# Optimization experiments

Hardware: AMD Instinct MI355X
Metric: run time of the kernel (lower is better)

Reference implementation:

```python
import jax, jax.numpy as jnp
import numpy as np


def _mlp(h, W1, b1, W2, b2):
    # Linear -> ReLU -> Linear
    h = jax.nn.relu(h @ W1 + b1)
    return h @ W2 + b2


def setup_inputs() -> dict:
    key = jax.random.key(0)
    ks = jax.random.split(key, 8)
    N, E, DN, DE, H, O = 50000, 800000, 128, 64, 256, 128
    DIN = DN + DE  # 192
    s1 = 1.0 / np.sqrt(DIN)
    s2 = 1.0 / np.sqrt(H)
    return {
        "x": jax.random.normal(ks[0], (N, DN), dtype=jnp.float32),
        "edge_index": jax.random.randint(ks[1], (2, E), 0, N, dtype=jnp.int32),
        "edge_attr": jax.random.normal(ks[2], (E, DE), dtype=jnp.float32),
        "W1_out": jax.random.normal(ks[3], (DIN, H), dtype=jnp.float32) * s1,
        "b1_out": jnp.zeros((H,), dtype=jnp.float32),
        "W2_out": jax.random.normal(ks[4], (H, O), dtype=jnp.float32) * s2,
        "b2_out": jnp.zeros((O,), dtype=jnp.float32),
        "W1_in": jax.random.normal(ks[5], (DIN, H), dtype=jnp.float32) * s1,
        "b1_in": jnp.zeros((H,), dtype=jnp.float32),
        "W2_in": jax.random.normal(ks[6], (H, O), dtype=jnp.float32) * s2,
        "b2_in": jnp.zeros((O,), dtype=jnp.float32),
    }


def reference(x, edge_index, edge_attr, W1_out, b1_out, W2_out, b2_out,
              W1_in, b1_in, W2_in, b2_in):
    N = x.shape[0]
    row, col = edge_index[0], edge_index[1]
    # Shared gather + concat: [E, d_node + d_edge]
    msg_in = jnp.concatenate([x[col], edge_attr], axis=1)

    # flow_out: edges with row < col. Compute MLP densely, zero masked edges,
    # then scatter-sum -> identical math to masked gather + scatter-sum.
    m_out = (row < col).astype(x.dtype)[:, None]
    flow_out = _mlp(msg_in, W1_out, b1_out, W2_out, b2_out) * m_out
    flow_out = jax.ops.segment_sum(flow_out, row, num_segments=N)

    # flow_in: edges with row > col
    m_in = (row > col).astype(x.dtype)[:, None]
    flow_in = _mlp(msg_in, W1_in, b1_in, W2_in, b2_in) * m_in
    flow_in = jax.ops.segment_sum(flow_in, row, num_segments=N)

    return jnp.concatenate((flow_in, flow_out), axis=1)  # [N, 2*O]
```

## Files before the change

### kernel.cpp

```cpp
#include <hip/hip_runtime.h>
#include <hip/hip_bf16.h>

typedef __attribute__((ext_vector_type(8))) short short8;
typedef __attribute__((ext_vector_type(8))) unsigned short ushort8;
typedef __attribute__((ext_vector_type(4))) float f32x4;
typedef __attribute__((ext_vector_type(2))) unsigned int uint2v;
typedef __attribute__((ext_vector_type(4))) unsigned int uint4v;

#define DN   128
#define DE   64
#define DIN  192
#define HID  256
#define OUTD 128
#define TE   64
#define NT   256
#define MSG_LD 200
#define OUT_LD 132
#define NMB  (TE / 16)

static __device__ __forceinline__ unsigned short f2b(float f) {
    unsigned int u = __float_as_uint(f);
    u += 0x7fffu + ((u >> 16) & 1u);
    return (unsigned short)(u >> 16);
}

static __device__ __forceinline__ unsigned int cvt_pk2(float lo, float hi) {
    unsigned int r;
    asm("v_cvt_pk_bf16_f32 %0, %1, %2" : "=v"(r) : "v"(lo), "v"(hi));
    return r;
}

template<int OFF>
static __device__ __forceinline__ uint2v tr_read(unsigned addr) {
    uint2v d;
    asm volatile("ds_read_b64_tr_b16 %0, %1 offset:%c2"
                 : "=v"(d) : "v"(addr), "n"(OFF));
    return d;
}

__global__ __launch_bounds__(256)
void prep_kernel(const float* __restrict__ W1o, const float* __restrict__ W1i,
                 const float* __restrict__ W2o, const float* __restrict__ W2i,
                 unsigned short* __restrict__ W1po, unsigned short* __restrict__ W1pi,
                 unsigned short* __restrict__ W2po, unsigned short* __restrict__ W2pi,
                 const int* __restrict__ ei, int E, int N, int* __restrict__ hist,
                 const float* __restrict__ x, unsigned short* __restrict__ xb) {
    const int S1 = DIN * HID, S2v = HID * OUTD;
    const int PACKN = 2 * S1 + 2 * S2v;
    int idx = blockIdx.x * blockDim.x + threadIdx.x;
    if (idx < PACKN) {
        const float* W; unsigned short* Wp; int Nc, j;
        if      (idx < S1)          { W = W1o; Wp = W1po; Nc = HID;  j = idx; }
        else if (idx < 2*S1)        { W = W1i; Wp = W1pi; Nc = HID;  j = idx - S1; }
        else if (idx < 2*S1 + S2v)  { W = W2o; Wp = W2po; Nc = OUTD; j = idx - 2*S1; }
        else                        { W = W2i; Wp = W2pi; Nc = OUTD; j = idx - 2*S1 - S2v; }
        int k = j / Nc, n = j - k * Nc;
        Wp[(((k >> 5) * Nc + n) << 5) + (k & 31)] = f2b(W[j]);
    } else if (idx < PACKN + E) {
        int e = idx - PACKN;
        int r = ei[e], c = ei[E + e];
        if      (r < c) atomicAdd(&hist[r], 1);
        else if (r > c) atomicAdd(&hist[N + r], 1);
    } else {
        int i = idx - PACKN - E;
        if (i < N * DN / 8) {
            float4 a = reinterpret_cast<const float4*>(x)[i * 2];
            float4 b = reinterpret_cast<const float4*>(x)[i * 2 + 1];
            ushort8 v = { f2b(a.x), f2b(a.y), f2b(a.z), f2b(a.w),
                          f2b(b.x), f2b(b.y), f2b(b.z), f2b(b.w) };
            reinterpret_cast<ushort8*>(xb)[i] = v;
        }
    }
}

__global__ __launch_bounds__(1024)
void scan1_kernel(const int* __restrict__ hist, int* __restrict__ cursor,
                  int* __restrict__ chunkSum, int N, int nch) {
    __shared__ int s_ws[16];
    const int br = blockIdx.x / nch, ch = blockIdx.x - br * nch;
    const int tid = threadIdx.x, lane = tid & 63, wv = tid >> 6;
    const int i = ch * 1024 + tid;
    int v = (i < N) ? hist[(size_t)br * N + i] : 0;
    int incl = v;
    #pragma unroll
    for (int d = 1; d < 64; d <<= 1) {
        int t = __shfl_up(incl, d, 64);
        if (lane >= d) incl += t;
    }
    if (lane == 63) s_ws[wv] = incl;
    __syncthreads();
    if (tid < 16) {
        int w = s_ws[tid];
        int wi = w;
        #pragma unroll
        for (int d = 1; d < 16; d <<= 1) {
            int t = __shfl_up(wi, d, 64);
            if (tid >= d) wi += t;
        }
        s_ws[tid] = wi - w;
    }
    __syncthreads();
    int excl = s_ws[wv] + incl - v;
    if (i < N) cursor[(size_t)br * N + i] = excl;
    if (tid == 1023) chunkSum[br * nch + ch] = excl + v;
}

__global__ __launch_bounds__(128)
void scan2_kernel(int* __restrict__ chunkSum, int* __restrict__ cnt, int nch) {
    const int br = threadIdx.x >> 6, lane = threadIdx.x & 63;
    int v = (lane < nch) ? chunkSum[br * nch + lane] : 0;
    int incl = v;
    #pragma unroll
    for (int d = 1; d < 64; d <<= 1) {
        int t = __shfl_up(incl, d, 64);
        if (lane >= d) incl += t;
    }
    if (lane < nch) chunkSum[br * nch + lane] = incl - v;
    if (lane == nch - 1) cnt[br] = incl;
}

__global__ __launch_bounds__(256)
void reorder_kernel(const int* __restrict__ ei, int E, int N, int nch,
                    int* __restrict__ cursor, const int* __restrict__ chunkSum,
                    int* __restrict__ list_out, int* __restrict__ list_in) {
    int e = blockIdx.x * blockDim.x + threadIdx.x;
    if (e >= E) return;
    int r = ei[e], c = ei[E + e];
    if (r == c) return;
    int br = (r < c) ? 0 : 1;
    int p = chunkSum[br * nch + (r >> 10)] + atomicAdd(&cursor[(size_t)br * N + r], 1);
    (br ? list_in : list_out)[p] = e;
}

__global__ __launch_bounds__(NT, 4)
void mlp_scatter_kernel(const unsigned short* __restrict__ xb,
                        const int* __restrict__ ei,
                        const float* __restrict__ ea,
                        const unsigned short* __restrict__ W1p_out,
                        const unsigned short* __restrict__ W1p_in,
                        const float* __restrict__ b1_out,
                        const float* __restrict__ b1_in,
                        const unsigned short* __restrict__ W2p_out,
                        const unsigned short* __restrict__ W2p_in,
                        const float* __restrict__ b2_out,
                        const float* __restrict__ b2_in,
                        const int* __restrict__ list_out,
                        const int* __restrict__ list_in,
                        const int* __restrict__ cnt,
                        float* __restrict__ out,
                        int E) {
    __shared__ __align__(16) unsigned short s_buf[TE * 264];
    __shared__ int s_eid[TE], s_dest[TE], s_col[TE];

    const int c0 = cnt[0], c1 = cnt[1];
    const int nb0 = (c0 + TE - 1) / TE;
    const int branch = (blockIdx.x >= nb0) ? 1 : 0;
    const int lb = branch ? (blockIdx.x - nb0) : blockIdx.x;
    const int count = branch ? c1 : c0;
    if (lb * TE >= count) return;
    const int* list            = branch ? list_in : list_out;
    const unsigned short* W1p  = branch ? W1p_in  : W1p_out;
    const float* b1            = branch ? b1_in   : b1_out;
    const unsigned short* W2p  = branch ? W2p_in  : W2p_out;
    const float* b2            = branch ? b2_in   : b2_out;
    const int colbase          = branch ? 0 : OUTD;

    const int tid = threadIdx.x;
    if (tid < TE) {
        int idx = lb * TE + tid;
        int e = (idx < count) ? list[idx] : -1;
        s_eid[tid]  = e;
        s_dest[tid] = (e >= 0) ? ei[e] : -1;
        s_col[tid]  = (e >= 0) ? ei[E + e] : 0;
    }
    __syncthreads();

    {
        const int le  = tid >> 2;
        const int sub = tid & 3;
        const int e   = s_eid[le];
        const ushort8* xrow = reinterpret_cast<const ushort8*>(xb) + (size_t)s_col[le] * (DN / 8);
        #pragma unroll
        for (int j = 0; j < 4; ++j) {
            int seg = sub + j * 4;
            ushort8 v = {0, 0, 0, 0, 0, 0, 0, 0};
            if (e >= 0) v = xrow[seg];
            *reinterpret_cast<ushort8*>(&s_buf[le * MSG_LD + seg * 8]) = v;
        }
        const float4* erow = reinterpret_cast<const float4*>(ea) + (size_t)e * (DE / 4);
        #pragma unroll
        for (int j = 0; j < 4; ++j) {
            float4 v = make_float4(0.f, 0.f, 0.f, 0.f);
            if (e >= 0) v = erow[sub * 4 + j];
            unsigned int lo = cvt_pk2(v.x, v.y);
            unsigned int hi = cvt_pk2(v.z, v.w);
            *reinterpret_cast<uint2*>(&s_buf[le * MSG_LD + DN + sub * 16 + j * 4]) = make_uint2(lo, hi);
        }
    }
    __syncthreads();

    const int wave = tid >> 6;
    const int lane = tid & 63;
    const int ln   = lane & 15;
    const int quad = lane >> 4;

    f32x4 acc[4][4];
    {
        const int nbase = wave * 64;
        float bias[4];
        #pragma unroll
        for (int t = 0; t < 4; ++t) bias[t] = b1[nbase + t * 16 + ln];
        #pragma unroll
        for (int mt = 0; mt < 4; ++mt)
            #pragma unroll
            for (int t = 0; t < 4; ++t)
                acc[mt][t] = (f32x4){bias[t], bias[t], bias[t], bias[t]};
        #pragma unroll
        for (int kt = 0; kt < DIN / 32; ++kt) {
            short8 a[4], b[4];
            #pragma unroll
            for (int mt = 0; mt < 4; ++mt)
                a[mt] = *reinterpret_cast<const short8*>(
                    &s_buf[(mt * 16 + ln) * MSG_LD + kt * 32 + quad * 8]);
            #pragma unroll
            for (int t = 0; t < 4; ++t)
                b[t] = *reinterpret_cast<const short8*>(
                    &W1p[((kt * HID + nbase + t * 16 + ln) << 5) + quad * 8]);
            #pragma unroll
            for (int mt = 0; mt < 4; ++mt)
                #pragma unroll
                for (int t = 0; t < 4; ++t)
                    acc[mt][t] = __builtin_amdgcn_mfma_f32_16x16x32_bf16(a[mt], b[t], acc[mt][t], 0, 0, 0);
        }
    }
    __syncthreads();

    {
        const int nbase = wave * 64;
        #pragma unroll
        for (int mt = 0; mt < 4; ++mt)
            #pragma unroll
            for (int t = 0; t < 4; ++t) {
                int n = nbase + t * 16 + ln;
                float r0 = acc[mt][t][0], r1 = acc[mt][t][1];
                float r2 = acc[mt][t][2], r3 = acc[mt][t][3];
                r0 = r0 > 0.f ? r0 : 0.f;  r1 = r1 > 0.f ? r1 : 0.f;
                r2 = r2 > 0.f ? r2 : 0.f;  r3 = r3 > 0.f ? r3 : 0.f;
                unsigned int d0 = cvt_pk2(r0, r1);
                unsigned int d1 = cvt_pk2(r2, r3);
                int el = (((n >> 2) * NMB + mt) << 6) + ((n & 3) << 4) + (quad << 2);
                *reinterpret_cast<uint2v*>(&s_buf[el]) = (uint2v){d0, d1};
            }
    }
    __syncthreads();

    f32x4 acc2[4][2];
    {
        const int nb2 = wave * 32;
        float bz0 = b2[nb2 + ln];
        float bz1 = b2[nb2 + 16 + ln];
        #pragma unroll
        for (int mt = 0; mt < 4; ++mt) {
            acc2[mt][0] = (f32x4){bz0, bz0, bz0, bz0};
            acc2[mt][1] = (f32x4){bz1, bz1, bz1, bz1};
        }
        const unsigned trb = (unsigned)(uintptr_t)(&s_buf[quad * 512 + ln * 4]);
        short8 bn0 = *reinterpret_cast<const short8*>(&W2p[((nb2 + ln) << 5) + quad * 8]);
        short8 bn1 = *reinterpret_cast<const short8*>(&W2p[((nb2 + 16 + ln) << 5) + quad * 8]);

#define G2TR(kt, mt) { \
        uint2v t0 = tr_read<(kt) * 4096 + (mt) * 128>(trb); \
        uint2v t1 = tr_read<(kt) * 4096 + (mt) * 128 + 512>(trb); \
        a[mt] = __builtin_bit_cast(short8, (uint4v){t0.x, t0.y, t1.x, t1.y}); }

#define G2MM(mt) \
        acc2[mt][0] = __builtin_amdgcn_mfma_f32_16x16x32_bf16(a[mt], b0c, acc2[mt][0], 0, 0, 0); \
        acc2[mt][1] = __builtin_amdgcn_mfma_f32_16x16x32_bf16(a[mt], b1c, acc2[mt][1], 0, 0, 0);

#define G2STEP(kt) { \
        short8 a[4]; \
        G2TR(kt, 0) G2TR(kt, 1) G2TR(kt, 2) G2TR(kt, 3) \
        short8 b0c = bn0, b1c = bn1; \
        if ((kt) < 7) { \
            bn0 = *reinterpret_cast<const short8*>(&W2p[((((kt) + 1) * OUTD + nb2 + ln) << 5) + quad * 8]); \
            bn1 = *reinterpret_cast<const short8*>(&W2p[((((kt) + 1) * OUTD + nb2 + 16 + ln) << 5) + quad * 8]); \
        } \
        asm volatile("s_waitcnt lgkmcnt(0)"); \
        __builtin_amdgcn_sched_barrier(0); \
        G2MM(0) G2MM(1) G2MM(2) G2MM(3) }

        G2STEP(0) G2STEP(1) G2STEP(2) G2STEP(3)
        G2STEP(4) G2STEP(5) G2STEP(6) G2STEP(7)
#undef G2STEP
#undef G2MM
#undef G2TR
    }
    __syncthreads();

    float* s_outf = reinterpret_cast<float*>(s_buf);
    {
        const int nb2 = wave * 32;
        #pragma unroll
        for (int mt = 0; mt < 4; ++mt)
            #pragma unroll
            for (int t = 0; t < 2; ++t)
                #pragma unroll
                for (int r = 0; r < 4; ++r)
                    s_outf[(mt * 16 + quad * 4 + r) * OUT_LD + nb2 + t * 16 + ln] = acc2[mt][t][r];
    }
    __syncthreads();

    {
        const int c  = tid & 127;
        const int m0 = (tid >> 7) * 32;
        float run = 0.f;
        int cur = -1, rs = m0;
        for (int m = m0; m < m0 + 32; ++m) {
            int d = s_dest[m];
            float v = s_outf[m * OUT_LD + c];
            if (d != cur) {
                if (cur >= 0) {
                    float* p = &out[(size_t)cur * (2 * OUTD) + colbase + c];
                    if (rs > m0) *p = run; else atomicAdd(p, run);
                }
                cur = d; run = 0.f; rs = m;
            }
            if (d >= 0) run += v;
        }
        if (cur >= 0)
            atomicAdd(&out[(size_t)cur * (2 * OUTD) + colbase + c], run);
    }
}

extern "C" void kernel_launch(void* const* d_in, const int* in_sizes, int n_in,
                              void* d_out, int out_size, void* d_ws, size_t ws_size,
                              hipStream_t stream) {
    const float* x   = (const float*)d_in[0];
    const int*   ei  = (const int*)d_in[1];
    const float* ea  = (const float*)d_in[2];
    const float* W1o = (const float*)d_in[3];
    const float* b1o = (const float*)d_in[4];
    const float* W2o = (const float*)d_in[5];
    const float* b2o = (const float*)d_in[6];
    const float* W1i = (const float*)d_in[7];
    const float* b1i = (const float*)d_in[8];
    const float* W2i = (const float*)d_in[9];
    const float* b2i = (const float*)d_in[10];
    float* out = (float*)d_out;
    const int E = in_sizes[1] / 2;
    const int N = in_sizes[0] / DN;
    const int nch = (N + 1023) >> 10;

    int* cnt      = (int*)d_ws;
    int* chunkSum = cnt + 16;
    int* hist     = chunkSum + 128;
    int* cursor   = hist + 2 * (size_t)N;
    int* list_out = cursor + 2 * (size_t)N;
    int* list_in  = list_out + E;
    unsigned short* W1po = (unsigned short*)(list_in + E);
    unsigned short* W1pi = W1po + DIN * HID;
    unsigned short* W2po = W1pi + DIN * HID;
    unsigned short* W2pi = W2po + HID * OUTD;
    unsigned short* xb   = W2pi + HID * OUTD;

    hipMemsetAsync(d_out, 0, (size_t)out_size * sizeof(float), stream);
    hipMemsetAsync(d_ws, 0, (576 + 8 * (size_t)N), stream);

    const int PACKN = 2 * DIN * HID + 2 * HID * OUTD;
    const int prepN = PACKN + E + N * DN / 8;
    prep_kernel<<<(prepN + 255) / 256, 256, 0, stream>>>(
        W1o, W1i, W2o, W2i, W1po, W1pi, W2po, W2pi, ei, E, N, hist, x, xb);

    scan1_kernel<<<2 * nch, 1024, 0, stream>>>(hist, cursor, chunkSum, N, nch);
    scan2_kernel<<<1, 128, 0, stream>>>(chunkSum, cnt, nch);
    reorder_kernel<<<(E + 255) / 256, 256, 0, stream>>>(
        ei, E, N, nch, cursor, chunkSum, list_out, list_in);

    const int nblk = (E + TE - 1) / TE + 2;
    mlp_scatter_kernel<<<nblk, NT, 0, stream>>>(
        xb, ei, ea, W1po, W1pi, b1o, b1i, W2po, W2pi, b2o, b2i,
        list_out, list_in, cnt, out, E);
}
```

Baseline: 573.7 us.

## Fuse scan kernels with last-block decoupled pass and vectorize small stores

Merges the two scan kernels into one, where the last block to finish (tracked by an atomic counter in the workspace) performs the chunk-sum scan, removing one kernel launch. Weight packing now iterates over the output index so packed writes are contiguous and reads are strided. Edge-attribute conversion writes 16-byte LDS stores instead of 8-byte ones, and the scatter epilogue has half the threads each handle two columns with float2 loads and stores. A workspace-size guard is also added. The scatter change halves the active threads in the epilogue, which may lengthen it.

After: 608.8 us. 6.1% more time.

```diff
diff --git a/kernel.cpp b/kernel.cpp
--- a/kernel.cpp
+++ b/kernel.cpp
@@ -49,13 +49,21 @@
     const int PACKN = 2 * S1 + 2 * S2v;
     int idx = blockIdx.x * blockDim.x + threadIdx.x;
     if (idx < PACKN) {
-        const float* W; unsigned short* Wp; int Nc, j;
-        if      (idx < S1)          { W = W1o; Wp = W1po; Nc = HID;  j = idx; }
-        else if (idx < 2*S1)        { W = W1i; Wp = W1pi; Nc = HID;  j = idx - S1; }
-        else if (idx < 2*S1 + S2v)  { W = W2o; Wp = W2po; Nc = OUTD; j = idx - 2*S1; }
-        else                        { W = W2i; Wp = W2pi; Nc = OUTD; j = idx - 2*S1 - S2v; }
-        int k = j / Nc, n = j - k * Nc;
-        Wp[(((k >> 5) * Nc + n) << 5) + (k & 31)] = f2b(W[j]);
+        if (idx < 2 * S1) {
+            const float* W = (idx < S1) ? W1o : W1i;
+            unsigned short* Wp = (idx < S1) ? W1po : W1pi;
+            int j = (idx < S1) ? idx : idx - S1;
+            int k5 = j & 31, t = j >> 5;
+            int n = t & (HID - 1), kq = t >> 8;
+            Wp[j] = f2b(W[(kq * 32 + k5) * HID + n]);
+        } else {
+            const float* W = (idx < 2 * S1 + S2v) ? W2o : W2i;
+            unsigned short* Wp = (idx < 2 * S1 + S2v) ? W2po : W2pi;
+            int j = (idx < 2 * S1 + S2v) ? idx - 2 * S1 : idx - 2 * S1 - S2v;
+            int k5 = j & 31, t = j >> 5;
+            int n = t & (OUTD - 1), kq = t >> 7;
+            Wp[j] = f2b(W[(kq * 32 + k5) * OUTD + n]);
+        }
     } else if (idx < PACKN + E) {
         int e = idx - PACKN;
         int r = ei[e], c = ei[E + e];
@@ -74,9 +82,11 @@
 }
 
 __global__ __launch_bounds__(1024)
-void scan1_kernel(const int* __restrict__ hist, int* __restrict__ cursor,
-                  int* __restrict__ chunkSum, int N, int nch) {
+void scan_kernel(const int* __restrict__ hist, int* __restrict__ cursor,
+                 int* __restrict__ chunkSum, int* __restrict__ cnt,
+                 int* __restrict__ done, int N, int nch) {
     __shared__ int s_ws[16];
+    __shared__ int s_flag;
     const int br = blockIdx.x / nch, ch = blockIdx.x - br * nch;
     const int tid = threadIdx.x, lane = tid & 63, wv = tid >> 6;
     const int i = ch * 1024 + tid;
@@ -102,21 +112,28 @@
     __syncthreads();
     int excl = s_ws[wv] + incl - v;
     if (i < N) cursor[(size_t)br * N + i] = excl;
-    if (tid == 1023) chunkSum[br * nch + ch] = excl + v;
-}
-
-__global__ __launch_bounds__(128)
-void scan2_kernel(int* __restrict__ chunkSum, int* __restrict__ cnt, int nch) {
-    const int br = threadIdx.x >> 6, lane = threadIdx.x & 63;
-    int v = (lane < nch) ? chunkSum[br * nch + lane] : 0;
-    int incl = v;
-    #pragma unroll
-    for (int d = 1; d < 64; d <<= 1) {
-        int t = __shfl_up(incl, d, 64);
-        if (lane >= d) incl += t;
-    }
-    if (lane < nch) chunkSum[br * nch + lane] = incl - v;
-    if (lane == nch - 1) cnt[br] = incl;
+    if (tid == 1023)
+        atomicExch(&chunkSum[br * nch + ch], excl + v);
+    __threadfence();
+    __syncthreads();
+    if (tid == 0) {
+        __threadfence();
+        int old = atomicAdd(done, 1);
+        s_flag = (old == (int)gridDim.x - 1) ? 1 : 0;
+    }
+    __syncthreads();
+    if (s_flag && tid < 128) {
+        const int fbr = tid >> 6, fl = tid & 63;
+        int v2 = (fl < nch) ? atomicAdd(&chunkSum[fbr * nch + fl], 0) : 0;
+        int inc2 = v2;
+        #pragma unroll
+        for (int d = 1; d < 64; d <<= 1) {
+            int t = __shfl_up(inc2, d, 64);
+            if (fl >= d) inc2 += t;
+        }
+        if (fl < nch) chunkSum[fbr * nch + fl] = inc2 - v2;
+        if (fl == nch - 1) cnt[fbr] = inc2;
+    }
 }
 
 __global__ __launch_bounds__(256)
@@ -189,12 +206,12 @@
         }
         const float4* erow = reinterpret_cast<const float4*>(ea) + (size_t)e * (DE / 4);
         #pragma unroll
-        for (int j = 0; j < 4; ++j) {
-            float4 v = make_float4(0.f, 0.f, 0.f, 0.f);
-            if (e >= 0) v = erow[sub * 4 + j];
-            unsigned int lo = cvt_pk2(v.x, v.y);
-            unsigned int hi = cvt_pk2(v.z, v.w);
-            *reinterpret_cast<uint2*>(&s_buf[le * MSG_LD + DN + sub * 16 + j * 4]) = make_uint2(lo, hi);
+        for (int jj = 0; jj < 2; ++jj) {
+            float4 v0 = make_float4(0.f, 0.f, 0.f, 0.f), v1 = v0;
+            if (e >= 0) { v0 = erow[sub * 4 + jj * 2]; v1 = erow[sub * 4 + jj * 2 + 1]; }
+            uint4v w = { cvt_pk2(v0.x, v0.y), cvt_pk2(v0.z, v0.w),
+                         cvt_pk2(v1.x, v1.y), cvt_pk2(v1.z, v1.w) };
+            *reinterpret_cast<uint4v*>(&s_buf[le * MSG_LD + DN + sub * 16 + jj * 8]) = w;
         }
     }
     __syncthreads();
@@ -310,25 +327,28 @@
     }
     __syncthreads();
 
-    {
-        const int c  = tid & 127;
-        const int m0 = (tid >> 7) * 32;
-        float run = 0.f;
+    if (tid < 128) {
+        const int c  = (tid & 63) * 2;
+        const int m0 = (tid >> 6) * 32;
+        float2 run = make_float2(0.f, 0.f);
         int cur = -1, rs = m0;
         for (int m = m0; m < m0 + 32; ++m) {
             int d = s_dest[m];
-            float v = s_outf[m * OUT_LD + c];
+            float2 v = *reinterpret_cast<const float2*>(&s_outf[m * OUT_LD + c]);
             if (d != cur) {
                 if (cur >= 0) {
                     float* p = &out[(size_t)cur * (2 * OUTD) + colbase + c];
-                    if (rs > m0) *p = run; else atomicAdd(p, run);
+                    if (rs > m0) *reinterpret_cast<float2*>(p) = run;
+                    else { atomicAdd(p, run.x); atomicAdd(p + 1, run.y); }
                 }
-                cur = d; run = 0.f; rs = m;
+                cur = d; run = make_float2(0.f, 0.f); rs = m;
             }
-            if (d >= 0) run += v;
-        }
-        if (cur >= 0)
-            atomicAdd(&out[(size_t)cur * (2 * OUTD) + colbase + c], run);
+            if (d >= 0) { run.x += v.x; run.y += v.y; }
+        }
+        if (cur >= 0) {
+            float* p = &out[(size_t)cur * (2 * OUTD) + colbase + c];
+            atomicAdd(p, run.x); atomicAdd(p + 1, run.y);
+        }
     }
 }
 
@@ -363,6 +383,11 @@
     unsigned short* W2pi = W2po + HID * OUTD;
     unsigned short* xb   = W2pi + HID * OUTD;
 
+    size_t need = (size_t)(144 + 4 * (size_t)N + 2 * (size_t)E) * 4
+                + (size_t)(2 * DIN * HID + 2 * HID * OUTD) * 2
+                + (size_t)N * DN * 2;
+    if (need > ws_size) return;
+
     hipMemsetAsync(d_out, 0, (size_t)out_size * sizeof(float), stream);
     hipMemsetAsync(d_ws, 0, (576 + 8 * (size_t)N), stream);
 
@@ -371,8 +396,7 @@
     prep_kernel<<<(prepN + 255) / 256, 256, 0, stream>>>(
         W1o, W1i, W2o, W2i, W1po, W1pi, W2po, W2pi, ei, E, N, hist, x, xb);
 
-    scan1_kernel<<<2 * nch, 1024, 0, stream>>>(hist, cursor, chunkSum, N, nch);
-    scan2_kernel<<<1, 128, 0, stream>>>(chunkSum, cnt, nch);
+    scan_kernel<<<2 * nch, 1024, 0, stream>>>(hist, cursor, chunkSum, cnt, cnt + 2, N, nch);
     reorder_kernel<<<(E + 255) / 256, 256, 0, stream>>>(
         ei, E, N, nch, cursor, chunkSum, list_out, list_in);
 
```
